# Performance work log

Measured on AMD Instinct MI355X. Metric: run time of the kernel, lower is better.

The kernel has to match this reference:

```python
import jax, jax.numpy as jnp
import numpy as np

N, D = 8192, 256
E = 65536


def setup_inputs() -> dict:
    key = jax.random.key(0)
    ks = jax.random.split(key, 16)
    s = 1.0 / np.sqrt(D)  # nn.Linear default init scale
    return {
        "x_mean": jax.random.normal(ks[0], (N, D), dtype=jnp.float32),
        "x_var": jax.random.uniform(ks[1], (N, D), dtype=jnp.float32),
        "edge_index": jax.random.randint(ks[2], (2, E), 0, N, dtype=jnp.int64),
        "edge_timestamps": jax.random.uniform(ks[3], (E,), dtype=jnp.float32),
        "Wq": jax.random.uniform(ks[4], (D, D), jnp.float32, -s, s),
        "bq": jax.random.uniform(ks[5], (D,), jnp.float32, -s, s),
        "Wk": jax.random.uniform(ks[6], (D, D), jnp.float32, -s, s),
        "bk": jax.random.uniform(ks[7], (D,), jnp.float32, -s, s),
        "Wv": jax.random.uniform(ks[8], (D, D), jnp.float32, -s, s),
        "bv": jax.random.uniform(ks[9], (D,), jnp.float32, -s, s),
        "Wo": jax.random.uniform(ks[10], (D, D), jnp.float32, -s, s),
        "bo": jax.random.uniform(ks[11], (D,), jnp.float32, -s, s),
        "Wvar": jax.random.uniform(ks[12], (D, D), jnp.float32, -s, s),
        "bvar": jax.random.uniform(ks[13], (D,), jnp.float32, -s, s),
    }


def reference(x_mean, x_var, edge_index, edge_timestamps,
              Wq, bq, Wk, bk, Wv, bv, Wo, bo, Wvar, bvar):
    # edge_index / edge_timestamps are accepted but unused (as in the original forward).
    head_dim = D // 4  # num_heads=4; heads are never split, only used for scale
    scale = head_dim ** -0.5

    q = x_mean @ Wq.T + bq  # [N, D]
    k = x_mean @ Wk.T + bk
    v = x_mean @ Wv.T + bv

    attn = jax.nn.softmax((q @ k.T) * scale, axis=-1)  # [N, N] (dropout: eval mode)

    out_mean = (attn @ v) @ Wo.T + bo  # [N, D]

    v_var = x_var @ Wvar.T + bvar
    out_var = (attn * attn) @ v_var  # squared weights against projected variance
    return out_mean, out_var
```

## Files before the change

kernel.cpp:

```cpp
#include <hip/hip_runtime.h>
#include <hip/hip_bf16.h>
#include <hip/hip_fp16.h>

#define DEV __device__ __forceinline__

typedef __attribute__((ext_vector_type(8))) _Float16 h8;
typedef __attribute__((ext_vector_type(4))) float floatx4;

DEV float bf2f(unsigned short b) { return __uint_as_float(((unsigned)b) << 16); }

DEV void async_ld16(const void* g, void* l) {
  __builtin_amdgcn_global_load_lds(
      (const __attribute__((address_space(1))) unsigned int*)g,
      (__attribute__((address_space(3))) unsigned int*)l, 16, 0, 0);
}

DEV int detect_bf16(const void* x_mean) {
  const unsigned* w = (const unsigned*)x_mean;
  unsigned v = w[threadIdx.x & 63];
  unsigned ex = (v >> 7) & 0xFFu;
  int vote = (ex >= 100u && ex <= 144u) ? 1 : 0;
  unsigned long long b = __ballot(vote);
  return __popcll(b) >= 48 ? 1 : 0;
}

DEV float load_elem(const void* p, int isbf, size_t i) {
  return isbf ? bf2f(((const unsigned short*)p)[i]) : ((const float*)p)[i];
}

DEV void stage8h(const void* src, int isbf, size_t idx, float scale, _Float16* dst) {
  h8 o;
  if (isbf) {
    const unsigned short* s = (const unsigned short*)src + idx;
#pragma unroll
    for (int j = 0; j < 8; ++j) o[j] = (_Float16)(bf2f(s[j]) * scale);
  } else {
    const float* f = (const float*)src + idx;
    float4 a = *(const float4*)f;
    float4 b = *(const float4*)(f + 4);
    o[0] = (_Float16)(a.x * scale); o[1] = (_Float16)(a.y * scale);
    o[2] = (_Float16)(a.z * scale); o[3] = (_Float16)(a.w * scale);
    o[4] = (_Float16)(b.x * scale); o[5] = (_Float16)(b.y * scale);
    o[6] = (_Float16)(b.z * scale); o[7] = (_Float16)(b.w * scale);
  }
  *(h8*)dst = o;
}

struct ProjArgs {
  const void* A[4];
  const void* B[4];
  const void* bias[4];
  _Float16* C[4];
  int fl_tpc[4];
  float scale[4];
  int bias_row[4];
  const void* xdet;
};

__global__ __launch_bounds__(256) void proj_kernel(ProjArgs p) {
  __shared__ __align__(16) char smem[34816];
  _Float16* As = (_Float16*)smem;
  _Float16* Bs = As + 4096;
  _Float16* Ts = (_Float16*)smem;
  int isbf = detect_bf16(p.xdet);
  int z = blockIdx.z;
  size_t i0, j0;
  if (z < 2) { i0 = (size_t)blockIdx.x * 128; j0 = (size_t)blockIdx.y * 128; }
  else       { i0 = (size_t)blockIdx.y * 128; j0 = (size_t)blockIdx.x * 128; }
  const void* A = p.A[z];
  const void* B = p.B[z];
  const void* bias = p.bias[z];
  const float scale = p.scale[z];
  const int bias_row = p.bias_row[z];
  const int tpc = p.fl_tpc[z];
  _Float16* C = p.C[z];
  const int t = threadIdx.x;
  const int lane = t & 63, wave = t >> 6;
  const int wr = wave >> 1, wc = wave & 1;
  const int q = lane >> 4, m = lane & 15;
  floatx4 acc[4][4] = {};
  for (int k0 = 0; k0 < 256; k0 += 32) {
#pragma unroll
    for (int it = 0; it < 2; ++it) {
      int e = it * 2048 + t * 8;
      int row = e >> 5, col = e & 31;
      stage8h(A, isbf, (i0 + row) * (size_t)256 + k0 + col, 1.f, &As[e]);
      stage8h(B, isbf, (j0 + row) * (size_t)256 + k0 + col, 1.f, &Bs[e]);
    }
    __syncthreads();
    h8 af[4], bfr[4];
#pragma unroll
    for (int r = 0; r < 4; ++r)
      af[r] = *(const h8*)&As[(wr * 64 + r * 16 + m) * 32 + q * 8];
#pragma unroll
    for (int c = 0; c < 4; ++c)
      bfr[c] = *(const h8*)&Bs[(wc * 64 + c * 16 + m) * 32 + q * 8];
#pragma unroll
    for (int r = 0; r < 4; ++r)
#pragma unroll
      for (int c = 0; c < 4; ++c)
        acc[r][c] = __builtin_amdgcn_mfma_f32_16x16x32_f16(af[r], bfr[c], acc[r][c], 0, 0, 0);
    __syncthreads();
  }
#pragma unroll
  for (int r = 0; r < 4; ++r)
#pragma unroll
    for (int c = 0; c < 4; ++c) {
      size_t col = j0 + wc * 64 + c * 16 + m;
      float bcol = bias_row ? 0.f : load_elem(bias, isbf, col);
#pragma unroll
      for (int g = 0; g < 4; ++g) {
        size_t row = i0 + wr * 64 + r * 16 + q * 4 + g;
        float val = acc[r][c][g] + bcol;
        if (bias_row) val += load_elem(bias, isbf, row);
        Ts[(wr * 64 + r * 16 + q * 4 + g) * 136 + wc * 64 + c * 16 + m] =
            (_Float16)(val * scale);
      }
    }
  __syncthreads();
  size_t ti0 = i0 >> 4, tj0 = j0 >> 5;
#pragma unroll
  for (int it = 0; it < 8; ++it) {
    int cch = it * 4 + wave;
    int ci = cch >> 2, ck = cch & 3;
    int il = ci * 16 + (lane & 15);
    int jl = ck * 32 + (lane >> 4) * 8;
    h8 v = *(const h8*)&Ts[il * 136 + jl];
    *(h8*)&C[((ti0 + ci) * (size_t)tpc + (tj0 + ck)) * 512 + lane * 8] = v;
  }
}

__global__ __launch_bounds__(256) void zero_rs_kernel(float* __restrict__ rs) {
  rs[blockIdx.x * 256 + threadIdx.x] = 0.f;
}
__global__ __launch_bounds__(256) void zero_acc_kernel(float* __restrict__ a,
                                                       float* __restrict__ b) {
  size_t i = ((size_t)blockIdx.x * 256 + threadIdx.x) * 4;
  float4 z = {0.f, 0.f, 0.f, 0.f};
  *(float4*)(a + i) = z;
  *(float4*)(b + i) = z;
}

__global__ __launch_bounds__(512, 2) void flash_kernel(
    const _Float16* __restrict__ qb, const _Float16* __restrict__ kb,
    const _Float16* __restrict__ vT, const _Float16* __restrict__ vvT,
    float* __restrict__ rs, float* __restrict__ otm, float* __restrict__ otv) {
  __shared__ __align__(16) _Float16 Qs[64 * 512];
  __shared__ __align__(16) _Float16 Ks[32 * 512];
  __shared__ __align__(16) _Float16 Ps[32 * 512];
  const int t = threadIdx.x;
  const int lane = t & 63, wave = t >> 6;
  const int hi = lane >> 4, m = lane & 15;
  const size_t bx = blockIdx.x;
  const int z = blockIdx.y;
  const int wq = wave >> 1, wk = wave & 1;
  const int wq2 = wave >> 2, wd = wave & 3;

#pragma unroll
  for (int it = 0; it < 8; ++it) {
    int tile = it * 8 + wave;
    async_ld16(&qb[((bx * 8 + (size_t)(tile >> 3)) * 8 + (tile & 7)) * 512 + lane * 8],
               &Qs[tile * 512 + lane * 8]);
  }
  floatx4 accm[4][4] = {}, accv[4][4] = {};
  float rsum[2][4] = {};
  const size_t kvRowBase = (size_t)z * 128;
  for (int kvt = 0; kvt < 16; ++kvt) {
    floatx4 s[2][4] = {};
    const size_t kvRow0 = kvRowBase + kvt * 8;
#pragma unroll
    for (int ko = 0; ko < 2; ++ko) {
#pragma unroll
      for (int it = 0; it < 4; ++it)
        async_ld16(&kb[((kvRow0 + wave) * 8 + (size_t)(ko * 4 + it)) * 512 + lane * 8],
                   &Ks[(wave * 4 + it) * 512 + lane * 8]);
      __syncthreads();
#pragma unroll
      for (int kt2 = 0; kt2 < 4; ++kt2) {
        h8 af[2], bf[4];
#pragma unroll
        for (int r = 0; r < 2; ++r)
          af[r] = *(const h8*)&Qs[((wq * 2 + r) * 8 + ko * 4 + kt2) * 512 + lane * 8];
#pragma unroll
        for (int c = 0; c < 4; ++c)
          bf[c] = *(const h8*)&Ks[((wk * 4 + c) * 4 + kt2) * 512 + lane * 8];
#pragma unroll
        for (int r = 0; r < 2; ++r)
#pragma unroll
          for (int c = 0; c < 4; ++c)
            s[r][c] = __builtin_amdgcn_mfma_f32_16x16x32_f16(af[r], bf[c], s[r][c], 0, 0, 0);
      }
      __syncthreads();
    }
#pragma unroll
    for (int r = 0; r < 2; ++r)
#pragma unroll
      for (int c = 0; c < 4; ++c) {
        int kst = wk * 2 + (c >> 1);
        int lp = hi * 4 + 16 * (2 * (c & 1) + (m >> 3));
        _Float16* dst = &Ps[((wq * 2 + r) * 4 + kst) * 512 + lp * 8 + (m & 7)];
#pragma unroll
        for (int g = 0; g < 4; ++g) {
          float e = __expf(fminf(s[r][c][g], 8.f)) * 0.015625f;
          rsum[r][g] += e;
          dst[g * 8] = (_Float16)e;
        }
      }
    __syncthreads();
    const size_t kvT0 = (size_t)z * 64 + kvt * 4;
#pragma unroll
    for (int ks = 0; ks < 4; ++ks) {
      h8 a[4], a2[4], b1[4], b2[4];
#pragma unroll
      for (int c = 0; c < 4; ++c) {
        size_t bo_ = ((size_t)(wd * 4 + c) * 256 + kvT0 + ks) * 512 + lane * 8;
        b1[c] = *(const h8*)&vT[bo_];
        b2[c] = *(const h8*)&vvT[bo_];
      }
#pragma unroll
      for (int r = 0; r < 4; ++r) {
        a[r] = *(const h8*)&Ps[((wq2 * 4 + r) * 4 + ks) * 512 + lane * 8];
        a2[r] = a[r] * a[r];
      }
#pragma unroll
      for (int r = 0; r < 4; ++r)
#pragma unroll
        for (int c = 0; c < 4; ++c) {
          accm[r][c] = __builtin_amdgcn_mfma_f32_16x16x32_f16(a[r], b1[c], accm[r][c], 0, 0, 0);
          accv[r][c] = __builtin_amdgcn_mfma_f32_16x16x32_f16(a2[r], b2[c], accv[r][c], 0, 0, 0);
        }
    }
  }
#pragma unroll
  for (int r = 0; r < 2; ++r)
#pragma unroll
    for (int g = 0; g < 4; ++g) {
      float part = rsum[r][g];
      part += __shfl_xor(part, 1);
      part += __shfl_xor(part, 2);
      part += __shfl_xor(part, 4);
      part += __shfl_xor(part, 8);
      if (m == 0)
        unsafeAtomicAdd(&rs[bx * 128 + wq * 32 + r * 16 + hi * 4 + g], part);
    }
#pragma unroll
  for (int r = 0; r < 4; ++r)
#pragma unroll
    for (int g = 0; g < 4; ++g) {
      size_t row = bx * 128 + wq2 * 64 + r * 16 + hi * 4 + g;
#pragma unroll
      for (int c = 0; c < 4; ++c) {
        size_t col = wd * 64 + c * 16 + m;
        unsafeAtomicAdd(&otm[row * 256 + col], accm[r][c][g]);
        unsafeAtomicAdd(&otv[row * 256 + col], accv[r][c][g]);
      }
    }
}

__global__ __launch_bounds__(256) void final_kernel(const float* __restrict__ ot,
                                                    const void* Wo, const void* bo,
                                                    const void* xdet,
                                                    const float* __restrict__ rs,
                                                    float* __restrict__ Cm,
                                                    float* __restrict__ otv) {
  __shared__ __align__(16) _Float16 As[64 * 32];
  __shared__ __align__(16) _Float16 Bs[128 * 32];
  int isbf = detect_bf16(xdet);
  const int t = threadIdx.x;
  const int lane = t & 63, wave = t >> 6;
  const int wr = wave >> 1, wc = wave & 1;
  const int q = lane >> 4, m = lane & 15;
  const size_t i0 = (size_t)blockIdx.x * 64, j0 = (size_t)blockIdx.y * 128;
  floatx4 acc[2][4] = {};
  for (int k0 = 0; k0 < 256; k0 += 32) {
    {
      int e = t * 8;
      int row = e >> 5, col = e & 31;
      stage8h(ot, 0, (i0 + row) * (size_t)256 + k0 + col, 1.f, &As[e]);
    }
#pragma unroll
    for (int it = 0; it < 2; ++it) {
      int e = it * 2048 + t * 8;
      int row = e >> 5, col = e & 31;
      stage8h(Wo, isbf, (j0 + row) * (size_t)256 + k0 + col, 1.f, &Bs[e]);
    }
    __syncthreads();
    h8 af[2], bfr[4];
#pragma unroll
    for (int r = 0; r < 2; ++r)
      af[r] = *(const h8*)&As[(wr * 32 + r * 16 + m) * 32 + q * 8];
#pragma unroll
    for (int c = 0; c < 4; ++c)
      bfr[c] = *(const h8*)&Bs[(wc * 64 + c * 16 + m) * 32 + q * 8];
#pragma unroll
    for (int r = 0; r < 2; ++r)
#pragma unroll
      for (int c = 0; c < 4; ++c)
        acc[r][c] = __builtin_amdgcn_mfma_f32_16x16x32_f16(af[r], bfr[c], acc[r][c], 0, 0, 0);
    __syncthreads();
  }
#pragma unroll
  for (int r = 0; r < 2; ++r)
#pragma unroll
    for (int g = 0; g < 4; ++g) {
      size_t row = i0 + wr * 32 + r * 16 + q * 4 + g;
      float inv = 1.f / rs[row];
#pragma unroll
      for (int c = 0; c < 4; ++c) {
        size_t col = j0 + wc * 64 + c * 16 + m;
        float bcol = load_elem(bo, isbf, col);
        Cm[row * 256 + col] = acc[r][c][g] * inv + bcol;
      }
    }
#pragma unroll
  for (int it = 0; it < 8; ++it) {
    int e = it * 256 + t;
    int row = e >> 5, cg = e & 31;
    size_t rrow = i0 + row;
    float inv = 1.f / rs[rrow];
    float inv2 = inv * inv;
    float4* pp = (float4*)&otv[rrow * 256 + j0 + cg * 4];
    float4 v = *pp;
    v.x *= inv2; v.y *= inv2; v.z *= inv2; v.w *= inv2;
    *pp = v;
  }
}

extern "C" void kernel_launch(void* const* d_in, const int* in_sizes, int n_in,
                              void* d_out, int out_size, void* d_ws, size_t ws_size,
                              hipStream_t stream) {
  const void* x_mean = d_in[0];
  const void* x_var  = d_in[1];
  const void* Wq   = d_in[4];
  const void* bq   = d_in[5];
  const void* Wk   = d_in[6];
  const void* bk   = d_in[7];
  const void* Wv   = d_in[8];
  const void* bv   = d_in[9];
  const void* Wo   = d_in[10];
  const void* bo   = d_in[11];
  const void* Wvar = d_in[12];
  const void* bvar = d_in[13];
  float* out = (float*)d_out;

  const size_t NE_S = 67108864;
  const size_t NE_P = 2097152;
  if (ws_size < (NE_S + 5 * NE_P) * 2) return;
  _Float16* w   = (_Float16*)d_ws;
  _Float16* qb  = w;
  _Float16* kb  = qb + NE_P;
  _Float16* vT  = kb + NE_P;
  _Float16* vvT = vT + NE_P;
  float* rs     = (float*)(vvT + NE_P);
  float* ot_f32 = rs + 8192;

  ProjArgs p;
  p.A[0] = x_mean; p.B[0] = Wq;     p.bias[0] = bq;   p.C[0] = qb;  p.fl_tpc[0] = 8;   p.scale[0] = 0.125f; p.bias_row[0] = 0;
  p.A[1] = x_mean; p.B[1] = Wk;     p.bias[1] = bk;   p.C[1] = kb;  p.fl_tpc[1] = 8;   p.scale[1] = 1.f;    p.bias_row[1] = 0;
  p.A[2] = Wv;     p.B[2] = x_mean; p.bias[2] = bv;   p.C[2] = vT;  p.fl_tpc[2] = 256; p.scale[2] = 1.f;    p.bias_row[2] = 1;
  p.A[3] = Wvar;   p.B[3] = x_var;  p.bias[3] = bvar; p.C[3] = vvT; p.fl_tpc[3] = 256; p.scale[3] = 1.f;    p.bias_row[3] = 1;
  p.xdet = x_mean;

  zero_rs_kernel<<<dim3(32), 256, 0, stream>>>(rs);
  zero_acc_kernel<<<dim3(2048), 256, 0, stream>>>(ot_f32, out + NE_P);
  proj_kernel<<<dim3(64, 2, 4), 256, 0, stream>>>(p);
  flash_kernel<<<dim3(64, 4), 512, 0, stream>>>(qb, kb, vT, vvT, rs, ot_f32, out + NE_P);
  final_kernel<<<dim3(128, 2), 256, 0, stream>>>(ot_f32, Wo, bo, x_mean, rs, out, out + NE_P);
}
```

Baseline: 301.9 us.

## Halve flash query tile to 64 rows, double grid, split PV/PVV MFMA loops

Each flash block now owns 64 query rows instead of 128, and the grid doubles to 128x4 blocks. Launch bounds rise to 4 blocks per CU and LDS use drops. The mean and variance P·V accumulations move into separate loops to shrink the live register set. The aim is more occupancy and parallelism on the many CUs. In exchange, each block rereads V/Vvar from global with half the reuse, and the extra blocks issue more atomic traffic.

```diff
diff --git a/kernel.cpp b/kernel.cpp
--- a/kernel.cpp
+++ b/kernel.cpp
@@ -141,32 +141,32 @@
   *(float4*)(b + i) = z;
 }
 
-__global__ __launch_bounds__(512, 2) void flash_kernel(
+__global__ __launch_bounds__(512, 4) void flash_kernel(
     const _Float16* __restrict__ qb, const _Float16* __restrict__ kb,
     const _Float16* __restrict__ vT, const _Float16* __restrict__ vvT,
     float* __restrict__ rs, float* __restrict__ otm, float* __restrict__ otv) {
-  __shared__ __align__(16) _Float16 Qs[64 * 512];
+  __shared__ __align__(16) _Float16 Qs[32 * 512];
   __shared__ __align__(16) _Float16 Ks[32 * 512];
-  __shared__ __align__(16) _Float16 Ps[32 * 512];
+  __shared__ __align__(16) _Float16 Ps[16 * 512];
   const int t = threadIdx.x;
   const int lane = t & 63, wave = t >> 6;
   const int hi = lane >> 4, m = lane & 15;
   const size_t bx = blockIdx.x;
   const int z = blockIdx.y;
-  const int wq = wave >> 1, wk = wave & 1;
+  const int wq = wave >> 2, wk = wave & 3;
   const int wq2 = wave >> 2, wd = wave & 3;
 
 #pragma unroll
-  for (int it = 0; it < 8; ++it) {
+  for (int it = 0; it < 4; ++it) {
     int tile = it * 8 + wave;
-    async_ld16(&qb[((bx * 8 + (size_t)(tile >> 3)) * 8 + (tile & 7)) * 512 + lane * 8],
+    async_ld16(&qb[((bx * 4 + (size_t)(tile >> 3)) * 8 + (tile & 7)) * 512 + lane * 8],
                &Qs[tile * 512 + lane * 8]);
   }
-  floatx4 accm[4][4] = {}, accv[4][4] = {};
+  floatx4 accm[2][4] = {}, accv[2][4] = {};
   float rsum[2][4] = {};
   const size_t kvRowBase = (size_t)z * 128;
   for (int kvt = 0; kvt < 16; ++kvt) {
-    floatx4 s[2][4] = {};
+    floatx4 s[2][2] = {};
     const size_t kvRow0 = kvRowBase + kvt * 8;
 #pragma unroll
     for (int ko = 0; ko < 2; ++ko) {
@@ -177,17 +177,17 @@
       __syncthreads();
 #pragma unroll
       for (int kt2 = 0; kt2 < 4; ++kt2) {
-        h8 af[2], bf[4];
+        h8 af[2], bf[2];
 #pragma unroll
         for (int r = 0; r < 2; ++r)
           af[r] = *(const h8*)&Qs[((wq * 2 + r) * 8 + ko * 4 + kt2) * 512 + lane * 8];
 #pragma unroll
-        for (int c = 0; c < 4; ++c)
-          bf[c] = *(const h8*)&Ks[((wk * 4 + c) * 4 + kt2) * 512 + lane * 8];
+        for (int c = 0; c < 2; ++c)
+          bf[c] = *(const h8*)&Ks[((wk * 2 + c) * 4 + kt2) * 512 + lane * 8];
 #pragma unroll
         for (int r = 0; r < 2; ++r)
 #pragma unroll
-          for (int c = 0; c < 4; ++c)
+          for (int c = 0; c < 2; ++c)
             s[r][c] = __builtin_amdgcn_mfma_f32_16x16x32_f16(af[r], bf[c], s[r][c], 0, 0, 0);
       }
       __syncthreads();
@@ -195,10 +195,9 @@
 #pragma unroll
     for (int r = 0; r < 2; ++r)
 #pragma unroll
-      for (int c = 0; c < 4; ++c) {
-        int kst = wk * 2 + (c >> 1);
-        int lp = hi * 4 + 16 * (2 * (c & 1) + (m >> 3));
-        _Float16* dst = &Ps[((wq * 2 + r) * 4 + kst) * 512 + lp * 8 + (m & 7)];
+      for (int c = 0; c < 2; ++c) {
+        int lp = hi * 4 + 16 * (2 * c + (m >> 3));
+        _Float16* dst = &Ps[((wq * 2 + r) * 4 + wk) * 512 + lp * 8 + (m & 7)];
 #pragma unroll
         for (int g = 0; g < 4; ++g) {
           float e = __expf(fminf(s[r][c][g], 8.f)) * 0.015625f;
@@ -210,25 +209,35 @@
     const size_t kvT0 = (size_t)z * 64 + kvt * 4;
 #pragma unroll
     for (int ks = 0; ks < 4; ++ks) {
-      h8 a[4], a2[4], b1[4], b2[4];
-#pragma unroll
-      for (int c = 0; c < 4; ++c) {
-        size_t bo_ = ((size_t)(wd * 4 + c) * 256 + kvT0 + ks) * 512 + lane * 8;
-        b1[c] = *(const h8*)&vT[bo_];
-        b2[c] = *(const h8*)&vvT[bo_];
-      }
-#pragma unroll
-      for (int r = 0; r < 4; ++r) {
-        a[r] = *(const h8*)&Ps[((wq2 * 4 + r) * 4 + ks) * 512 + lane * 8];
-        a2[r] = a[r] * a[r];
-      }
-#pragma unroll
-      for (int r = 0; r < 4; ++r)
-#pragma unroll
-        for (int c = 0; c < 4; ++c) {
+      h8 a[2], b1[4];
+#pragma unroll
+      for (int c = 0; c < 4; ++c)
+        b1[c] = *(const h8*)&vT[((size_t)(wd * 4 + c) * 256 + kvT0 + ks) * 512 + lane * 8];
+#pragma unroll
+      for (int r = 0; r < 2; ++r)
+        a[r] = *(const h8*)&Ps[((wq2 * 2 + r) * 4 + ks) * 512 + lane * 8];
+#pragma unroll
+      for (int r = 0; r < 2; ++r)
+#pragma unroll
+        for (int c = 0; c < 4; ++c)
           accm[r][c] = __builtin_amdgcn_mfma_f32_16x16x32_f16(a[r], b1[c], accm[r][c], 0, 0, 0);
+    }
+#pragma unroll
+    for (int ks = 0; ks < 4; ++ks) {
+      h8 a2[2], b2[4];
+#pragma unroll
+      for (int c = 0; c < 4; ++c)
+        b2[c] = *(const h8*)&vvT[((size_t)(wd * 4 + c) * 256 + kvT0 + ks) * 512 + lane * 8];
+#pragma unroll
+      for (int r = 0; r < 2; ++r) {
+        h8 a = *(const h8*)&Ps[((wq2 * 2 + r) * 4 + ks) * 512 + lane * 8];
+        a2[r] = a * a;
+      }
+#pragma unroll
+      for (int r = 0; r < 2; ++r)
+#pragma unroll
+        for (int c = 0; c < 4; ++c)
           accv[r][c] = __builtin_amdgcn_mfma_f32_16x16x32_f16(a2[r], b2[c], accv[r][c], 0, 0, 0);
-        }
     }
   }
 #pragma unroll
@@ -241,13 +250,13 @@
       part += __shfl_xor(part, 4);
       part += __shfl_xor(part, 8);
       if (m == 0)
-        unsafeAtomicAdd(&rs[bx * 128 + wq * 32 + r * 16 + hi * 4 + g], part);
-    }
-#pragma unroll
-  for (int r = 0; r < 4; ++r)
+        unsafeAtomicAdd(&rs[bx * 64 + wq * 32 + r * 16 + hi * 4 + g], part);
+    }
+#pragma unroll
+  for (int r = 0; r < 2; ++r)
 #pragma unroll
     for (int g = 0; g < 4; ++g) {
-      size_t row = bx * 128 + wq2 * 64 + r * 16 + hi * 4 + g;
+      size_t row = bx * 64 + wq2 * 32 + r * 16 + hi * 4 + g;
 #pragma unroll
       for (int c = 0; c < 4; ++c) {
         size_t col = wd * 64 + c * 16 + m;
@@ -364,6 +373,6 @@
   zero_rs_kernel<<<dim3(32), 256, 0, stream>>>(rs);
   zero_acc_kernel<<<dim3(2048), 256, 0, stream>>>(ot_f32, out + NE_P);
   proj_kernel<<<dim3(64, 2, 4), 256, 0, stream>>>(p);
-  flash_kernel<<<dim3(64, 4), 512, 0, stream>>>(qb, kb, vT, vvT, rs, ot_f32, out + NE_P);
+  flash_kernel<<<dim3(128, 4), 512, 0, stream>>>(qb, kb, vT, vvT, rs, ot_f32, out + NE_P);
   final_kernel<<<dim3(128, 2), 256, 0, stream>>>(ot_f32, Wo, bo, x_mean, rs, out, out + NE_P);
 }
```

Result: slower. 336.2 us (+11.4%).

## Read K fragments directly from global, double-buffer P, remap blocks per XCD

Applied to the files above, without the earlier changes.

Drops the LDS staging of K tiles and their two barriers per half-tile, loading MFMA B-fragments straight from global memory instead. The P tile is double-buffered so the next iteration's writes don't need a barrier against the previous PV reads. The grid is flattened and remapped so blocks sharing a KV split land on the same XCD, aiming for better L2 reuse of K/V. The risk is more global load latency per MFMA and redundant K reads across waves without LDS sharing.

```diff
diff --git a/kernel.cpp b/kernel.cpp
--- a/kernel.cpp
+++ b/kernel.cpp
@@ -146,13 +146,14 @@
     const _Float16* __restrict__ vT, const _Float16* __restrict__ vvT,
     float* __restrict__ rs, float* __restrict__ otm, float* __restrict__ otv) {
   __shared__ __align__(16) _Float16 Qs[64 * 512];
-  __shared__ __align__(16) _Float16 Ks[32 * 512];
-  __shared__ __align__(16) _Float16 Ps[32 * 512];
+  __shared__ __align__(16) _Float16 Ps[2][32 * 512];
   const int t = threadIdx.x;
   const int lane = t & 63, wave = t >> 6;
   const int hi = lane >> 4, m = lane & 15;
-  const size_t bx = blockIdx.x;
-  const int z = blockIdx.y;
+  const int wid = blockIdx.x;
+  const int xcd = wid & 7;
+  const int z = xcd >> 1;
+  const size_t bx = (size_t)((xcd & 1) * 32 + (wid >> 3));
   const int wq = wave >> 1, wk = wave & 1;
   const int wq2 = wave >> 2, wd = wave & 3;
 
@@ -162,43 +163,36 @@
     async_ld16(&qb[((bx * 8 + (size_t)(tile >> 3)) * 8 + (tile & 7)) * 512 + lane * 8],
                &Qs[tile * 512 + lane * 8]);
   }
+  __syncthreads();
+
   floatx4 accm[4][4] = {}, accv[4][4] = {};
   float rsum[2][4] = {};
-  const size_t kvRowBase = (size_t)z * 128;
   for (int kvt = 0; kvt < 16; ++kvt) {
     floatx4 s[2][4] = {};
-    const size_t kvRow0 = kvRowBase + kvt * 8;
-#pragma unroll
-    for (int ko = 0; ko < 2; ++ko) {
-#pragma unroll
-      for (int it = 0; it < 4; ++it)
-        async_ld16(&kb[((kvRow0 + wave) * 8 + (size_t)(ko * 4 + it)) * 512 + lane * 8],
-                   &Ks[(wave * 4 + it) * 512 + lane * 8]);
-      __syncthreads();
-#pragma unroll
-      for (int kt2 = 0; kt2 < 4; ++kt2) {
-        h8 af[2], bf[4];
-#pragma unroll
-        for (int r = 0; r < 2; ++r)
-          af[r] = *(const h8*)&Qs[((wq * 2 + r) * 8 + ko * 4 + kt2) * 512 + lane * 8];
+    const size_t kvRow0 = (size_t)z * 128 + kvt * 8;
+#pragma unroll
+    for (int kt = 0; kt < 8; ++kt) {
+      h8 af[2], bf[4];
+#pragma unroll
+      for (int r = 0; r < 2; ++r)
+        af[r] = *(const h8*)&Qs[((wq * 2 + r) * 8 + kt) * 512 + lane * 8];
+#pragma unroll
+      for (int c = 0; c < 4; ++c)
+        bf[c] = *(const h8*)&kb[((kvRow0 + wk * 4 + c) * 8 + kt) * 512 + lane * 8];
+#pragma unroll
+      for (int r = 0; r < 2; ++r)
 #pragma unroll
         for (int c = 0; c < 4; ++c)
-          bf[c] = *(const h8*)&Ks[((wk * 4 + c) * 4 + kt2) * 512 + lane * 8];
-#pragma unroll
-        for (int r = 0; r < 2; ++r)
-#pragma unroll
-          for (int c = 0; c < 4; ++c)
-            s[r][c] = __builtin_amdgcn_mfma_f32_16x16x32_f16(af[r], bf[c], s[r][c], 0, 0, 0);
-      }
-      __syncthreads();
-    }
+          s[r][c] = __builtin_amdgcn_mfma_f32_16x16x32_f16(af[r], bf[c], s[r][c], 0, 0, 0);
+    }
+    _Float16* Pc = Ps[kvt & 1];
 #pragma unroll
     for (int r = 0; r < 2; ++r)
 #pragma unroll
       for (int c = 0; c < 4; ++c) {
         int kst = wk * 2 + (c >> 1);
         int lp = hi * 4 + 16 * (2 * (c & 1) + (m >> 3));
-        _Float16* dst = &Ps[((wq * 2 + r) * 4 + kst) * 512 + lp * 8 + (m & 7)];
+        _Float16* dst = &Pc[((wq * 2 + r) * 4 + kst) * 512 + lp * 8 + (m & 7)];
 #pragma unroll
         for (int g = 0; g < 4; ++g) {
           float e = __expf(fminf(s[r][c][g], 8.f)) * 0.015625f;
@@ -219,7 +213,7 @@
       }
 #pragma unroll
       for (int r = 0; r < 4; ++r) {
-        a[r] = *(const h8*)&Ps[((wq2 * 4 + r) * 4 + ks) * 512 + lane * 8];
+        a[r] = *(const h8*)&Pc[((wq2 * 4 + r) * 4 + ks) * 512 + lane * 8];
         a2[r] = a[r] * a[r];
       }
 #pragma unroll
@@ -364,6 +358,6 @@
   zero_rs_kernel<<<dim3(32), 256, 0, stream>>>(rs);
   zero_acc_kernel<<<dim3(2048), 256, 0, stream>>>(ot_f32, out + NE_P);
   proj_kernel<<<dim3(64, 2, 4), 256, 0, stream>>>(p);
-  flash_kernel<<<dim3(64, 4), 512, 0, stream>>>(qb, kb, vT, vvT, rs, ot_f32, out + NE_P);
+  flash_kernel<<<dim3(256), 512, 0, stream>>>(qb, kb, vT, vvT, rs, ot_f32, out + NE_P);
   final_kernel<<<dim3(128, 2), 256, 0, stream>>>(ot_f32, Wo, bo, x_mean, rs, out, out + NE_P);
 }
```

New measurement: 310.4 us. +2.8%, slower.
